# Kernel tuning notes

Measured on AMD Instinct MI355X. Metric: run time of the kernel, lower is better.

Reference implementation:

```python
import jax, jax.numpy as jnp
import numpy as np

CROP_H = 7
CROP_W = 7
EXTRAP = 0.0  # module hardcodes 0 when calling CropAndResizeFunction


def _crop_and_resize(image, boxes, box_ind):
    """TF-style crop_and_resize.
    image: (N,C,H,W) float; boxes: (M,4) normalized (y1,x1,y2,x2); box_ind: (M,) int32.
    Returns (M,C,CROP_H,CROP_W).
    """
    N, C, H, W = image.shape
    dt = image.dtype
    y1, x1, y2, x2 = boxes[:, 0], boxes[:, 1], boxes[:, 2], boxes[:, 3]
    ii = jnp.arange(CROP_H, dtype=dt)
    jj = jnp.arange(CROP_W, dtype=dt)
    # sample coordinates in feature-map space, shape (M, CROP_H) / (M, CROP_W)
    y = y1[:, None] * (H - 1) + ii[None, :] * ((y2 - y1) * (H - 1) / (CROP_H - 1))[:, None]
    x = x1[:, None] * (W - 1) + jj[None, :] * ((x2 - x1) * (W - 1) / (CROP_W - 1))[:, None]
    valid_y = (y >= 0) & (y <= H - 1)
    valid_x = (x >= 0) & (x <= W - 1)
    yt_f = jnp.floor(y)
    xt_f = jnp.floor(x)
    y_lerp = y - yt_f  # (M, oh)
    x_lerp = x - xt_f  # (M, ow)
    yt = jnp.clip(yt_f, 0, H - 1).astype(jnp.int32)
    yb = jnp.clip(jnp.ceil(y), 0, H - 1).astype(jnp.int32)
    xl = jnp.clip(xt_f, 0, W - 1).astype(jnp.int32)
    xr = jnp.clip(jnp.ceil(x), 0, W - 1).astype(jnp.int32)
    img = jnp.transpose(image, (0, 2, 3, 1))  # (N,H,W,C) for clean gather
    b = box_ind[:, None, None]                # (M,1,1)
    tl = img[b, yt[:, :, None], xl[:, None, :]]  # (M,oh,ow,C)
    tr = img[b, yt[:, :, None], xr[:, None, :]]
    bl = img[b, yb[:, :, None], xl[:, None, :]]
    br = img[b, yb[:, :, None], xr[:, None, :]]
    xl_w = x_lerp[:, None, :, None]
    top = tl + (tr - tl) * xl_w
    bot = bl + (br - bl) * xl_w
    out = top + (bot - top) * y_lerp[:, :, None, None]
    valid = (valid_y[:, :, None] & valid_x[:, None, :])[..., None]
    out = jnp.where(valid, out, jnp.asarray(EXTRAP, dt))
    return jnp.transpose(out, (0, 3, 1, 2))  # (M,C,oh,ow)


def setup_inputs() -> dict:
    key = jax.random.key(0)
    k0, k1, k2, k3, k4, k5 = jax.random.split(key, 6)
    N, C, H, W = 2, 256, 200, 304
    M = 2048
    scale = 0.0625  # 1/16
    Himg, Wimg = H / scale, W / scale
    featuremap = jax.random.normal(k0, (N, C, H, W), dtype=jnp.float32)
    x1 = jax.random.uniform(k1, (M, 1), minval=0.0, maxval=Wimg - 260.0)
    y1 = jax.random.uniform(k2, (M, 1), minval=0.0, maxval=Himg - 260.0)
    bw = jax.random.uniform(k3, (M, 1), minval=32.0, maxval=256.0)
    bh = jax.random.uniform(k4, (M, 1), minval=32.0, maxval=256.0)
    ids = jax.random.randint(k5, (M, 1), 0, N).astype(jnp.float32)
    rois = jnp.concatenate([ids, x1, y1, x1 + bw, y1 + bh], axis=1)
    return {"featuremap": featuremap, "rois": rois, "spatial_scale": jnp.float32(scale)}


def reference(featuremap, rois, spatial_scale):
    H, W = featuremap.shape[2], featuremap.shape[3]
    boxes = rois[:, 1:5] * spatial_scale
    box_ind = rois[:, 0].astype(jnp.int32)
    x1, y1, x2, y2 = boxes[:, 0], boxes[:, 1], boxes[:, 2], boxes[:, 3]
    spacing_w = (x2 - x1) / CROP_W
    spacing_h = (y2 - y1) / CROP_H
    nx0 = (x1 + spacing_w / 2 - 0.5) / (W - 1)
    ny0 = (y1 + spacing_h / 2 - 0.5) / (H - 1)
    nw = spacing_w * (CROP_W - 1) / (W - 1)
    nh = spacing_h * (CROP_H - 1) / (H - 1)
    boxes_n = jnp.stack([ny0, nx0, ny0 + nh, nx0 + nw], axis=1)
    return _crop_and_resize(featuremap, boxes_n, box_ind)
```

## Files before the change

kernel.cpp:

```cpp
#include <hip/hip_runtime.h>

#define RA_C   256
#define RA_H   200
#define RA_W   304
#define RA_HW  (RA_H * RA_W)
#define RA_CHW (RA_C * RA_HW)
#define CROPN  7
#define CROP2  (CROPN * CROPN)
#define OUT_M  (RA_C * CROP2)
#define BC     8
#define BB     2
#define REG_R  16
#define REG_C  20
#define NF4    5
#define CH_STR (REG_R * REG_C + 4)

__global__ __launch_bounds__(256) void roialign_kernel(
    const float* __restrict__ fm, const float* __restrict__ rois,
    const float* __restrict__ scale_p, float* __restrict__ out)
{
    __shared__ __align__(16) float s_reg[BB * BC * CH_STR];
    __shared__ int   s_yt[BB][CROPN], s_yb[BB][CROPN];
    __shared__ int   s_xl[BB][CROPN], s_xr[BB][CROPN];
    __shared__ float s_ylerp[BB][CROPN], s_vy[BB][CROPN];
    __shared__ float s_xlerp[BB][CROPN], s_vx[BB][CROPN];

    const int t = threadIdx.x;

    const int bid   = blockIdx.x;
    const int numBG = gridDim.x >> 5;
    const int xcd   = bid & 7;
    const int r     = bid >> 3;
    const int cgl   = r / numBG;
    const int bg    = r - cgl * numBG;
    const int m0    = bg * BB;
    const int c0    = (xcd * 4 + cgl) * BC;

    const int bx = t >> 7;
    const float scale = scale_p[0];
    const float* __restrict__ rr = rois + (size_t)(m0 + bx) * 5;

    int ys, xs, base;
    {
        #pragma clang fp contract(off)
        float ylo = rr[2] * scale, yhi = rr[4] * scale;
        float xlo = rr[1] * scale, xhi = rr[3] * scale;
        float spy = (yhi - ylo) / 7.0f;
        float n0y = (ylo + spy * 0.5f - 0.5f) / 199.0f;
        float cy  = n0y * 199.0f;
        float spx = (xhi - xlo) / 7.0f;
        float n0x = (xlo + spx * 0.5f - 0.5f) / 303.0f;
        float cx  = n0x * 303.0f;
        ys = (int)fminf(fmaxf(floorf(cy), 0.0f), 199.0f);
        xs = ((int)fminf(fmaxf(floorf(cx), 0.0f), 303.0f)) & ~3;
        base = (int)rr[0] * RA_CHW + c0 * RA_HW;
    }

    const int u   = t & 127;
    const int cc  = u >> 4;
    const int l16 = u & 15;
    const float* __restrict__ cp = fm + (size_t)(base + cc * RA_HW);
    float4 v[NF4];
    #pragma unroll
    for (int s = 0; s < NF4; ++s) {
        const int idx = l16 + (s << 4);
        const int r2  = idx / 5;
        const int kk  = idx - r2 * 5;
        const int row = min(ys + r2, RA_H - 1);
        const int col = min(xs + (kk << 2), RA_W - 4);
        v[s] = *reinterpret_cast<const float4*>(cp + row * RA_W + col);
    }

    if (t < BB * 2 * CROPN) {
        #pragma clang fp contract(off)
        {
            const int mm  = t / (2 * CROPN);
            const int k14 = t - mm * (2 * CROPN);
            const int axis = (k14 >= CROPN) ? 1 : 0;
            const int k = axis ? (k14 - CROPN) : k14;
            const float* __restrict__ rg = rois + (size_t)(m0 + mm) * 5;
            float lo, hi, szm1;
            if (axis == 0) { lo = rg[2] * scale; hi = rg[4] * scale; szm1 = (float)(RA_H - 1); }
            else           { lo = rg[1] * scale; hi = rg[3] * scale; szm1 = (float)(RA_W - 1); }
            float sp   = (hi - lo) / 7.0f;
            float n0   = (lo + sp * 0.5f - 0.5f) / szm1;
            float nsz  = sp * 6.0f / szm1;
            float b2   = n0 + nsz;
            float d    = (b2 - n0) * szm1 / 6.0f;
            float coord = n0 * szm1 + (float)k * d;
            float fl = floorf(coord);
            float ce = ceilf(coord);
            float lerp = coord - fl;
            int lo_i = (int)fminf(fmaxf(fl, 0.0f), szm1);
            int hi_i = (int)fminf(fmaxf(ce, 0.0f), szm1);
            float valid = (coord >= 0.0f && coord <= szm1) ? 1.0f : 0.0f;
            if (axis == 0) {
                s_yt[mm][k] = lo_i; s_yb[mm][k] = hi_i;
                s_ylerp[mm][k] = lerp; s_vy[mm][k] = valid;
            } else {
                s_xl[mm][k] = lo_i; s_xr[mm][k] = hi_i;
                s_xlerp[mm][k] = lerp; s_vx[mm][k] = valid;
            }
        }
    }

    {
        float* __restrict__ sp_ = s_reg + (bx * BC + cc) * CH_STR;
        #pragma unroll
        for (int s = 0; s < NF4; ++s) {
            const int idx = l16 + (s << 4);
            *reinterpret_cast<float4*>(sp_ + (idx << 2)) = v[s];
        }
    }
    __syncthreads();

    const int ij  = t & 63;
    const int chg = (t >> 6) & 1;
    if (ij < CROP2) {
        const int i = ij / CROPN;
        const int j = ij - i * CROPN;
        const int rT = min(s_yt[bx][i] - ys, REG_R - 1);
        const int rB = min(s_yb[bx][i] - ys, REG_R - 1);
        const int cl = min(s_xl[bx][j] - xs, REG_C - 1);
        const int cr = min(s_xr[bx][j] - xs, REG_C - 1);
        const float yw = s_ylerp[bx][i];
        const float xw = s_xlerp[bx][j];
        const float vv = s_vy[bx][i] * s_vx[bx][j];
        const int oT = rT * REG_C;
        const int oB = rB * REG_C;
        float* __restrict__ op =
            out + (size_t)(m0 + bx) * OUT_M + (size_t)(c0 + chg * 4) * CROP2 + ij;
        #pragma unroll
        for (int q = 0; q < 4; ++q) {
            const float* __restrict__ sp2 =
                s_reg + (bx * BC + chg * 4 + q) * CH_STR;
            const float tl = sp2[oT + cl];
            const float tr = sp2[oT + cr];
            const float bl = sp2[oB + cl];
            const float br = sp2[oB + cr];
            const float top = tl + (tr - tl) * xw;
            const float bot = bl + (br - bl) * xw;
            op[q * CROP2] = (top + (bot - top) * yw) * vv;
        }
    }
}

extern "C" void kernel_launch(void* const* d_in, const int* in_sizes, int n_in,
                              void* d_out, int out_size, void* d_ws, size_t ws_size,
                              hipStream_t stream) {
    const float* fm    = (const float*)d_in[0];
    const float* rois  = (const float*)d_in[1];
    const float* scale = (const float*)d_in[2];
    float* out = (float*)d_out;
    const int M = in_sizes[1] / 5;
    const int numBG = M / BB;
    roialign_kernel<<<dim3(32 * numBG), dim3(256), 0, stream>>>(fm, rois, scale, out);
}
```

Measured before the change: 268.4 us.

## Precompute per-ROI sampling geometry in a separate kernel and reuse via workspace

Moves the per-ROI coordinate, lerp and validity computation into a small pre-pass kernel that writes a 64-int record per ROI into the workspace. The main kernel then loads ys/xs/base and the table from that record instead of recomputing it in each of the 32 channel-group blocks per ROI. This cuts redundant divides and float math in the main kernel, but adds a second launch and a dependent global load before the feature-map gather can start.

```diff
diff --git a/kernel.cpp b/kernel.cpp
--- a/kernel.cpp
+++ b/kernel.cpp
@@ -14,16 +14,63 @@
 #define REG_C  20
 #define NF4    5
 #define CH_STR (REG_R * REG_C + 4)
+#define GREC   64
+
+__global__ __launch_bounds__(256) void geom_kernel(
+    const float* __restrict__ rois, const float* __restrict__ scale_p,
+    int* __restrict__ ws, int M)
+{
+    const int gid = blockIdx.x * 256 + threadIdx.x;
+    if (gid >= M * 2 * CROPN) return;
+    {
+        #pragma clang fp contract(off)
+        const int m   = gid / (2 * CROPN);
+        const int k14 = gid - m * (2 * CROPN);
+        int* __restrict__ rec = ws + (size_t)m * GREC;
+        const int axis = (k14 >= CROPN) ? 1 : 0;
+        const int k = axis ? (k14 - CROPN) : k14;
+        const float scale = scale_p[0];
+        const float* __restrict__ rr = rois + (size_t)m * 5;
+        float lo, hi, szm1;
+        if (axis == 0) { lo = rr[2] * scale; hi = rr[4] * scale; szm1 = (float)(RA_H - 1); }
+        else           { lo = rr[1] * scale; hi = rr[3] * scale; szm1 = (float)(RA_W - 1); }
+        float sp   = (hi - lo) / 7.0f;
+        float n0   = (lo + sp * 0.5f - 0.5f) / szm1;
+        float nsz  = sp * 6.0f / szm1;
+        float b2   = n0 + nsz;
+        float d    = (b2 - n0) * szm1 / 6.0f;
+        float coord = n0 * szm1 + (float)k * d;
+        float fl = floorf(coord);
+        float ce = ceilf(coord);
+        float lerp = coord - fl;
+        int lo_i = (int)fminf(fmaxf(fl, 0.0f), szm1);
+        int hi_i = (int)fminf(fmaxf(ce, 0.0f), szm1);
+        float valid = (coord >= 0.0f && coord <= szm1) ? 1.0f : 0.0f;
+        if (axis == 0) {
+            rec[k]      = lo_i;
+            rec[7 + k]  = hi_i;
+            rec[28 + k] = __float_as_int(lerp);
+            rec[35 + k] = __float_as_int(valid);
+            if (k == 0) {
+                rec[56] = lo_i;
+                rec[58] = (int)rr[0] * RA_CHW;
+            }
+        } else {
+            rec[14 + k] = lo_i;
+            rec[21 + k] = hi_i;
+            rec[42 + k] = __float_as_int(lerp);
+            rec[49 + k] = __float_as_int(valid);
+            if (k == 0) rec[57] = lo_i & ~3;
+        }
+    }
+}
 
 __global__ __launch_bounds__(256) void roialign_kernel(
-    const float* __restrict__ fm, const float* __restrict__ rois,
-    const float* __restrict__ scale_p, float* __restrict__ out)
+    const float* __restrict__ fm, const int* __restrict__ ws,
+    float* __restrict__ out)
 {
     __shared__ __align__(16) float s_reg[BB * BC * CH_STR];
-    __shared__ int   s_yt[BB][CROPN], s_yb[BB][CROPN];
-    __shared__ int   s_xl[BB][CROPN], s_xr[BB][CROPN];
-    __shared__ float s_ylerp[BB][CROPN], s_vy[BB][CROPN];
-    __shared__ float s_xlerp[BB][CROPN], s_vx[BB][CROPN];
+    __shared__ int s_tab[BB][GREC];
 
     const int t = threadIdx.x;
 
@@ -37,24 +84,11 @@
     const int c0    = (xcd * 4 + cgl) * BC;
 
     const int bx = t >> 7;
-    const float scale = scale_p[0];
-    const float* __restrict__ rr = rois + (size_t)(m0 + bx) * 5;
+    const int* __restrict__ rec = ws + (size_t)(m0 + bx) * GREC;
 
-    int ys, xs, base;
-    {
-        #pragma clang fp contract(off)
-        float ylo = rr[2] * scale, yhi = rr[4] * scale;
-        float xlo = rr[1] * scale, xhi = rr[3] * scale;
-        float spy = (yhi - ylo) / 7.0f;
-        float n0y = (ylo + spy * 0.5f - 0.5f) / 199.0f;
-        float cy  = n0y * 199.0f;
-        float spx = (xhi - xlo) / 7.0f;
-        float n0x = (xlo + spx * 0.5f - 0.5f) / 303.0f;
-        float cx  = n0x * 303.0f;
-        ys = (int)fminf(fmaxf(floorf(cy), 0.0f), 199.0f);
-        xs = ((int)fminf(fmaxf(floorf(cx), 0.0f), 303.0f)) & ~3;
-        base = (int)rr[0] * RA_CHW + c0 * RA_HW;
-    }
+    const int ys   = rec[56];
+    const int xs   = rec[57];
+    const int base = rec[58] + c0 * RA_HW;
 
     const int u   = t & 127;
     const int cc  = u >> 4;
@@ -71,37 +105,10 @@
         v[s] = *reinterpret_cast<const float4*>(cp + row * RA_W + col);
     }
 
-    if (t < BB * 2 * CROPN) {
-        #pragma clang fp contract(off)
-        {
-            const int mm  = t / (2 * CROPN);
-            const int k14 = t - mm * (2 * CROPN);
-            const int axis = (k14 >= CROPN) ? 1 : 0;
-            const int k = axis ? (k14 - CROPN) : k14;
-            const float* __restrict__ rg = rois + (size_t)(m0 + mm) * 5;
-            float lo, hi, szm1;
-            if (axis == 0) { lo = rg[2] * scale; hi = rg[4] * scale; szm1 = (float)(RA_H - 1); }
-            else           { lo = rg[1] * scale; hi = rg[3] * scale; szm1 = (float)(RA_W - 1); }
-            float sp   = (hi - lo) / 7.0f;
-            float n0   = (lo + sp * 0.5f - 0.5f) / szm1;
-            float nsz  = sp * 6.0f / szm1;
-            float b2   = n0 + nsz;
-            float d    = (b2 - n0) * szm1 / 6.0f;
-            float coord = n0 * szm1 + (float)k * d;
-            float fl = floorf(coord);
-            float ce = ceilf(coord);
-            float lerp = coord - fl;
-            int lo_i = (int)fminf(fmaxf(fl, 0.0f), szm1);
-            int hi_i = (int)fminf(fmaxf(ce, 0.0f), szm1);
-            float valid = (coord >= 0.0f && coord <= szm1) ? 1.0f : 0.0f;
-            if (axis == 0) {
-                s_yt[mm][k] = lo_i; s_yb[mm][k] = hi_i;
-                s_ylerp[mm][k] = lerp; s_vy[mm][k] = valid;
-            } else {
-                s_xl[mm][k] = lo_i; s_xr[mm][k] = hi_i;
-                s_xlerp[mm][k] = lerp; s_vx[mm][k] = valid;
-            }
-        }
+    if (t < BB * GREC) {
+        const int b = t >> 6;
+        const int w = t & 63;
+        s_tab[b][w] = ws[(size_t)(m0 + b) * GREC + w];
     }
 
     {
@@ -119,13 +126,15 @@
     if (ij < CROP2) {
         const int i = ij / CROPN;
         const int j = ij - i * CROPN;
-        const int rT = min(s_yt[bx][i] - ys, REG_R - 1);
-        const int rB = min(s_yb[bx][i] - ys, REG_R - 1);
-        const int cl = min(s_xl[bx][j] - xs, REG_C - 1);
-        const int cr = min(s_xr[bx][j] - xs, REG_C - 1);
-        const float yw = s_ylerp[bx][i];
-        const float xw = s_xlerp[bx][j];
-        const float vv = s_vy[bx][i] * s_vx[bx][j];
+        const int rT = min(s_tab[bx][i]      - ys, REG_R - 1);
+        const int rB = min(s_tab[bx][7 + i]  - ys, REG_R - 1);
+        const int cl = min(s_tab[bx][14 + j] - xs, REG_C - 1);
+        const int cr = min(s_tab[bx][21 + j] - xs, REG_C - 1);
+        const float yw = __int_as_float(s_tab[bx][28 + i]);
+        const float vy = __int_as_float(s_tab[bx][35 + i]);
+        const float xw = __int_as_float(s_tab[bx][42 + j]);
+        const float vx = __int_as_float(s_tab[bx][49 + j]);
+        const float vv = vy * vx;
         const int oT = rT * REG_C;
         const int oB = rB * REG_C;
         float* __restrict__ op =
@@ -152,7 +161,12 @@
     const float* rois  = (const float*)d_in[1];
     const float* scale = (const float*)d_in[2];
     float* out = (float*)d_out;
+    int* ws = (int*)d_ws;
     const int M = in_sizes[1] / 5;
     const int numBG = M / BB;
-    roialign_kernel<<<dim3(32 * numBG), dim3(256), 0, stream>>>(fm, rois, scale, out);
+
+    const int gthreads = M * 2 * CROPN;
+    geom_kernel<<<dim3((gthreads + 255) / 256), dim3(256), 0, stream>>>(
+        rois, scale, ws, M);
+    roialign_kernel<<<dim3(32 * numBG), dim3(256), 0, stream>>>(fm, ws, out);
 }
```

Result: no change. 273.6 us (+1.9%).
